# Kernel optimization log

Hardware: AMD Instinct MI355X
Metric: run time of the kernel (lower is better)

The kernel has to match this reference:

```python
import jax, jax.numpy as jnp
import numpy as np

D_MODEL = 2048
N_HEADS = 16
D_HEAD = D_MODEL // N_HEADS
FF = 4 * D_MODEL
ROPE_BASE = 10000.0


def setup_inputs() -> dict:
    key = jax.random.key(0)
    ks = jax.random.split(key, 12)
    s = 0.02
    B, S = 2, 2048
    return {
        "x": jax.random.normal(ks[0], (B, S, D_MODEL), dtype=jnp.float32),
        # torch Linear layout: [out_features, in_features]
        "w_qkv": jax.random.normal(ks[1], (3 * D_MODEL, D_MODEL), dtype=jnp.float32) * s,
        "w_proj": jax.random.normal(ks[2], (D_MODEL, D_MODEL), dtype=jnp.float32) * s,
        "b_proj": jnp.zeros((D_MODEL,), dtype=jnp.float32),
        "w_ff1": jax.random.normal(ks[3], (FF, D_MODEL), dtype=jnp.float32) * s,
        "b_ff1": jnp.zeros((FF,), dtype=jnp.float32),
        "w_ff2": jax.random.normal(ks[4], (D_MODEL, FF), dtype=jnp.float32) * s,
        "b_ff2": jnp.zeros((D_MODEL,), dtype=jnp.float32),
        "g1": jnp.ones((D_MODEL,), dtype=jnp.float32),
        "beta1": jnp.zeros((D_MODEL,), dtype=jnp.float32),
        "g2": jnp.ones((D_MODEL,), dtype=jnp.float32),
        "beta2": jnp.zeros((D_MODEL,), dtype=jnp.float32),
    }


def _layer_norm(x, g, b, eps=1e-5):
    mu = jnp.mean(x, axis=-1, keepdims=True)
    var = jnp.var(x, axis=-1, keepdims=True)
    return (x - mu) * jax.lax.rsqrt(var + eps) * g + b


def _rope_cos_sin(seq_len, dtype):
    inv_freq = 1.0 / (ROPE_BASE ** (jnp.arange(0, D_HEAD, 2, dtype=jnp.float32) / D_HEAD))
    t = jnp.arange(seq_len, dtype=jnp.float32)
    freqs = jnp.einsum("i,j->ij", t, inv_freq)  # [S, D_HEAD//2]
    emb = jnp.concatenate([freqs, freqs], axis=-1)  # [S, D_HEAD]
    return jnp.cos(emb).astype(dtype), jnp.sin(emb).astype(dtype)


def _rotate_half(x):
    x1, x2 = x[..., : D_HEAD // 2], x[..., D_HEAD // 2 :]
    return jnp.concatenate([-x2, x1], axis=-1)


def reference(x, w_qkv, w_proj, b_proj, w_ff1, b_ff1, w_ff2, b_ff2, g1, beta1, g2, beta2):
    B, S, _ = x.shape
    # --- attention block ---
    h = _layer_norm(x, g1, beta1)
    qkv = h @ w_qkv.T  # [B,S,3D]
    xq, xk, xv = jnp.split(qkv, 3, axis=-1)
    xq = xq.reshape(B, S, N_HEADS, D_HEAD)
    xk = xk.reshape(B, S, N_HEADS, D_HEAD)
    xv = xv.reshape(B, S, N_HEADS, D_HEAD)
    cos, sin = _rope_cos_sin(S, x.dtype)
    cos = cos[None, :, None, :]  # [1,S,1,Dh]
    sin = sin[None, :, None, :]
    xq = xq * cos + _rotate_half(xq) * sin
    xk = xk * cos + _rotate_half(xk) * sin
    # SDPA, causal
    scale = 1.0 / jnp.sqrt(jnp.asarray(D_HEAD, dtype=x.dtype))
    scores = jnp.einsum("bqhd,bkhd->bhqk", xq, xk) * scale  # [B,H,S,S]
    causal = jnp.tril(jnp.ones((S, S), dtype=bool))
    scores = jnp.where(causal[None, None], scores, jnp.finfo(x.dtype).min)
    att = jax.nn.softmax(scores, axis=-1)
    out = jnp.einsum("bhqk,bkhd->bqhd", att, xv).reshape(B, S, D_MODEL)
    att_out = out @ w_proj.T + b_proj
    x = x + att_out
    # --- feed-forward block (exact GELU, matching nn.GELU default) ---
    h = _layer_norm(x, g2, beta2)
    ff = jax.nn.gelu(h @ w_ff1.T + b_ff1, approximate=False) @ w_ff2.T + b_ff2
    return x + ff
```

## Files before the change

kernel.cpp:

```cpp
#include <hip/hip_runtime.h>
#include <hip/hip_bf16.h>
#include <cmath>

#define D_MODEL 2048
#define N_HEADS 16
#define D_HEAD  128
#define FFDIM   8192
#define BATCH   2
#define SEQ     2048
#define TOKENS  (BATCH * SEQ)

using bf16 = __hip_bfloat16;
typedef __bf16 v8bf  __attribute__((ext_vector_type(8)));
typedef float  v4f   __attribute__((ext_vector_type(4)));
typedef float  v16f  __attribute__((ext_vector_type(16)));

#define N0 (3 * D_MODEL * D_MODEL / 4)
#define N1 (D_MODEL * D_MODEL / 4)
#define N2 (FFDIM * D_MODEL / 4)
#define N3 (D_MODEL * FFDIM / 4)

__global__ __launch_bounds__(256) void cast4_kernel(const float* __restrict__ w0,
                                                    const float* __restrict__ w1,
                                                    const float* __restrict__ w2,
                                                    const float* __restrict__ w3,
                                                    bf16* __restrict__ o0,
                                                    bf16* __restrict__ o1,
                                                    bf16* __restrict__ o2,
                                                    bf16* __restrict__ o3) {
    int i = blockIdx.x * 256 + threadIdx.x;
    const float* src; bf16* dst; int j;
    if (i < N0)                { src = w0; dst = o0; j = i; }
    else if (i < N0 + N1)      { src = w1; dst = o1; j = i - N0; }
    else if (i < N0 + N1 + N2) { src = w2; dst = o2; j = i - N0 - N1; }
    else                       { src = w3; dst = o3; j = i - N0 - N1 - N2; }
    float4 f = ((const float4*)src)[j];
    int o = j * 4;
    dst[o + 0] = __float2bfloat16(f.x);
    dst[o + 1] = __float2bfloat16(f.y);
    dst[o + 2] = __float2bfloat16(f.z);
    dst[o + 3] = __float2bfloat16(f.w);
}

__global__ __launch_bounds__(256) void ln_kernel(const float* __restrict__ x,
                                                 const float* __restrict__ g,
                                                 const float* __restrict__ b,
                                                 bf16* __restrict__ out) {
    int row = blockIdx.x;
    int t = threadIdx.x;
    const float* xr = x + (size_t)row * D_MODEL;
    float v[8];
    float s = 0.f, s2 = 0.f;
#pragma unroll
    for (int i = 0; i < 8; i++) {
        float val = xr[t + 256 * i];
        v[i] = val;
        s += val;
        s2 += val * val;
    }
#pragma unroll
    for (int off = 32; off > 0; off >>= 1) {
        s  += __shfl_down(s, off, 64);
        s2 += __shfl_down(s2, off, 64);
    }
    __shared__ float ws1[4], ws2[4];
    int wv = t >> 6;
    if ((t & 63) == 0) { ws1[wv] = s; ws2[wv] = s2; }
    __syncthreads();
    float fs  = ws1[0] + ws1[1] + ws1[2] + ws1[3];
    float fs2 = ws2[0] + ws2[1] + ws2[2] + ws2[3];
    float mean = fs * (1.0f / D_MODEL);
    float var  = fs2 * (1.0f / D_MODEL) - mean * mean;
    float rstd = rsqrtf(var + 1e-5f);
    bf16* orow = out + (size_t)row * D_MODEL;
#pragma unroll
    for (int i = 0; i < 8; i++) {
        int c = t + 256 * i;
        orow[c] = __float2bfloat16((v[i] - mean) * rstd * g[c] + b[c]);
    }
}

__global__ __launch_bounds__(256) void rope_kernel(bf16* __restrict__ qkv) {
    int unit = blockIdx.x * 4 + (threadIdx.x >> 6);
    int j = threadIdx.x & 63;
    int h = unit & (N_HEADS - 1);
    int tok = unit >> 4;
    int pos = tok & (SEQ - 1);
    float invf = powf(10000.0f, -(float)j / 64.0f);
    float ang = (float)pos * invf;
    float c = cosf(ang), s = sinf(ang);
    const float sc = 0.08838834764831845f;
    size_t base = (size_t)tok * (3 * D_MODEL) + h * D_HEAD;
    float q1 = __bfloat162float(qkv[base + j]), q2 = __bfloat162float(qkv[base + j + 64]);
    qkv[base + j]      = __float2bfloat16((q1 * c - q2 * s) * sc);
    qkv[base + j + 64] = __float2bfloat16((q2 * c + q1 * s) * sc);
    size_t kb = base + D_MODEL;
    float k1 = __bfloat162float(qkv[kb + j]), k2 = __bfloat162float(qkv[kb + j + 64]);
    qkv[kb + j]      = __float2bfloat16(k1 * c - k2 * s);
    qkv[kb + j + 64] = __float2bfloat16(k2 * c + k1 * s);
}

__global__ __launch_bounds__(256) void vt_kernel(const bf16* __restrict__ qkv,
                                                 bf16* __restrict__ vt) {
    __shared__ float tile[32][65];
    int bh = blockIdx.x;
    int k0 = blockIdx.y * 64;
    int d0 = blockIdx.z * 32;
    int b = bh >> 4, h = bh & 15;
    int t = threadIdx.x;
    const bf16* src = qkv + ((size_t)b * SEQ + k0) * (3 * D_MODEL) + 2 * D_MODEL + h * D_HEAD + d0;
#pragma unroll
    for (int i = 0; i < 8; i++) {
        int e = t + 256 * i;
        int kr = e >> 5, dc = e & 31;
        tile[dc][kr] = __bfloat162float(src[(size_t)kr * (3 * D_MODEL) + dc]);
    }
    __syncthreads();
    bf16* dst = vt + ((size_t)bh * D_HEAD + d0) * SEQ + k0;
#pragma unroll
    for (int i = 0; i < 8; i++) {
        int e = t + 256 * i;
        int dr = e >> 6, kc = e & 63;
        dst[(size_t)dr * SEQ + kc] = __float2bfloat16(tile[dr][kc]);
    }
}

#define KS_STRIDE 136
#define VT_STRIDE 72
#define PS_STRIDE 72

__global__ __launch_bounds__(256) void flash_attn(const bf16* __restrict__ qkv,
                                                  const bf16* __restrict__ vt,
                                                  bf16* __restrict__ att) {
    __shared__ __align__(16) bf16 Ks[64 * KS_STRIDE];
    __shared__ __align__(16) bf16 Vts[D_HEAD * VT_STRIDE];
    __shared__ __align__(16) bf16 Ps[4 * 16 * PS_STRIDE];

    int bh = blockIdx.x;
    int qt = (int)gridDim.y - 1 - (int)blockIdx.y;
    int b = bh >> 4, h = bh & 15;
    int t = threadIdx.x, wave = t >> 6, lane = t & 63;
    int lr = lane & 15, lq = lane >> 4;

    const bf16* qp = qkv + ((size_t)b * SEQ + qt * 64 + wave * 16 + lr) * (3 * D_MODEL) + h * D_HEAD;
    v8bf aq[4];
#pragma unroll
    for (int c = 0; c < 4; c++)
        aq[c] = *(const v8bf*)(qp + c * 32 + lq * 8);

    float m_r[4], l_r[4];
    v4f O[8] = {};
#pragma unroll
    for (int r = 0; r < 4; r++) { m_r[r] = -1e30f; l_r[r] = 0.f; }

    int n_tiles = qt + 1;
    for (int kt = 0; kt < n_tiles; kt++) {
        int kv0 = kt * 64;
        __syncthreads();
        {
            const bf16* kbase = qkv + ((size_t)b * SEQ + kv0) * (3 * D_MODEL) + D_MODEL + h * D_HEAD;
#pragma unroll
            for (int i = 0; i < 4; i++) {
                int e = t + 256 * i;
                int kr = e >> 4, c8 = (e & 15) * 8;
                *(uint4*)&Ks[kr * KS_STRIDE + c8] = *(const uint4*)(kbase + (size_t)kr * (3 * D_MODEL) + c8);
            }
            const bf16* vbase = vt + (size_t)bh * D_HEAD * SEQ + kv0;
#pragma unroll
            for (int i = 0; i < 4; i++) {
                int e8 = t + 256 * i;
                int dr = e8 >> 3, k8 = (e8 & 7) * 8;
                *(uint4*)&Vts[dr * VT_STRIDE + k8] = *(const uint4*)(vbase + (size_t)dr * SEQ + k8);
            }
        }
        __syncthreads();

        v4f sc[4];
#pragma unroll
        for (int nt = 0; nt < 4; nt++) {
            v4f a = {};
#pragma unroll
            for (int c = 0; c < 4; c++) {
                v8bf bk = *(const v8bf*)&Ks[(nt * 16 + lr) * KS_STRIDE + c * 32 + lq * 8];
                a = __builtin_amdgcn_mfma_f32_16x16x32_bf16(aq[c], bk, a, 0, 0, 0);
            }
            sc[nt] = a;
        }
        if (kt == n_tiles - 1) {
#pragma unroll
            for (int nt = 0; nt < 4; nt++)
#pragma unroll
                for (int r = 0; r < 4; r++) {
                    int cl = nt * 16 + lr, rl = wave * 16 + lq * 4 + r;
                    if (cl > rl) sc[nt][r] = -1e30f;
                }
        }
        float mt[4];
#pragma unroll
        for (int r = 0; r < 4; r++) {
            float v = fmaxf(fmaxf(sc[0][r], sc[1][r]), fmaxf(sc[2][r], sc[3][r]));
#pragma unroll
            for (int mk = 8; mk >= 1; mk >>= 1) v = fmaxf(v, __shfl_xor(v, mk, 64));
            mt[r] = v;
        }
        float alpha[4];
#pragma unroll
        for (int r = 0; r < 4; r++) {
            float mn = fmaxf(m_r[r], mt[r]);
            alpha[r] = __expf(m_r[r] - mn);
            m_r[r] = mn;
        }
        bf16* pw = &Ps[wave * 16 * PS_STRIDE];
        float rs[4] = {0.f, 0.f, 0.f, 0.f};
#pragma unroll
        for (int nt = 0; nt < 4; nt++)
#pragma unroll
            for (int r = 0; r < 4; r++) {
                float p = __expf(sc[nt][r] - m_r[r]);
                rs[r] += p;
                pw[(lq * 4 + r) * PS_STRIDE + nt * 16 + lr] = __float2bfloat16(p);
            }
#pragma unroll
        for (int r = 0; r < 4; r++) {
            float v = rs[r];
#pragma unroll
            for (int mk = 8; mk >= 1; mk >>= 1) v += __shfl_xor(v, mk, 64);
            l_r[r] = l_r[r] * alpha[r] + v;
        }
#pragma unroll
        for (int jt = 0; jt < 8; jt++)
#pragma unroll
            for (int r = 0; r < 4; r++) O[jt][r] *= alpha[r];

        asm volatile("s_waitcnt lgkmcnt(0)" ::: "memory");

        v8bf ap[2];
#pragma unroll
        for (int c = 0; c < 2; c++)
            ap[c] = *(const v8bf*)&pw[lr * PS_STRIDE + c * 32 + lq * 8];
#pragma unroll
        for (int jt = 0; jt < 8; jt++) {
#pragma unroll
            for (int c = 0; c < 2; c++) {
                v8bf bv = *(const v8bf*)&Vts[(jt * 16 + lr) * VT_STRIDE + c * 32 + lq * 8];
                O[jt] = __builtin_amdgcn_mfma_f32_16x16x32_bf16(ap[c], bv, O[jt], 0, 0, 0);
            }
        }
    }

    float inv[4];
#pragma unroll
    for (int r = 0; r < 4; r++) inv[r] = 1.0f / l_r[r];
#pragma unroll
    for (int jt = 0; jt < 8; jt++)
#pragma unroll
        for (int r = 0; r < 4; r++) {
            size_t idx = ((size_t)b * SEQ + qt * 64 + wave * 16 + lq * 4 + r) * D_MODEL + h * D_HEAD + jt * 16 + lr;
            att[idx] = __float2bfloat16(O[jt][r] * inv[r]);
        }
}

#define BM 128
#define BN 128
#define BK 64

template <int EPI>
__global__ __launch_bounds__(256) void gemm_bt(const bf16* __restrict__ A,
                                               const bf16* __restrict__ W,
                                               const float* __restrict__ bias,
                                               const float* __restrict__ res,
                                               float* __restrict__ outF,
                                               bf16* __restrict__ outB,
                                               int M, int N, int K) {
    __shared__ __align__(16) bf16 As[BM * BK];
    __shared__ __align__(16) bf16 Bs[BN * BK];
    int t = threadIdx.x;
    int wave = t >> 6, lane = t & 63;
    int wm = (wave >> 1) * 64;
    int wn = (wave & 1) * 64;
    int l31 = lane & 31;
    int kh  = lane >> 5;

    int nbx = gridDim.x;
    int bid = (int)blockIdx.y * nbx + (int)blockIdx.x;
    int per = (nbx * (int)gridDim.y) >> 3;
    int lbid = (bid & 7) * per + (bid >> 3);
    const int GM = 8;
    int pw = GM * nbx;
    int panel = lbid / pw;
    int rem = lbid - panel * pw;
    int bm = panel * GM + (rem & (GM - 1));
    int bn = rem >> 3;
    int row0 = bm * BM;
    int col0 = bn * BN;

    int srow = lane >> 3;
    int sblk = lane & 7;
    int scol = ((sblk ^ srow) * 8);

    v16f acc[2][2] = {};

    for (int k0 = 0; k0 < K; k0 += BK) {
#pragma unroll
        for (int u = 0; u < 4; u++) {
            int c = wave * 4 + u;
            const bf16* ga = A + (size_t)(row0 + c * 8 + srow) * K + k0 + scol;
            __builtin_amdgcn_global_load_lds(
                (const __attribute__((address_space(1))) void*)ga,
                (__attribute__((address_space(3))) void*)&As[c * 512], 16, 0, 0);
            const bf16* gb = W + (size_t)(col0 + c * 8 + srow) * K + k0 + scol;
            __builtin_amdgcn_global_load_lds(
                (const __attribute__((address_space(1))) void*)gb,
                (__attribute__((address_space(3))) void*)&Bs[c * 512], 16, 0, 0);
        }
        __syncthreads();
#pragma unroll
        for (int ks = 0; ks < 4; ks++) {
            int soff = (((ks * 2 + kh) ^ (lane & 7)) * 8);
            v8bf a0 = *(const v8bf*)(&As[(wm +      l31) * BK + soff]);
            v8bf a1 = *(const v8bf*)(&As[(wm + 32 + l31) * BK + soff]);
            v8bf b0 = *(const v8bf*)(&Bs[(wn +      l31) * BK + soff]);
            v8bf b1 = *(const v8bf*)(&Bs[(wn + 32 + l31) * BK + soff]);
            acc[0][0] = __builtin_amdgcn_mfma_f32_32x32x16_bf16(a0, b0, acc[0][0], 0, 0, 0);
            acc[0][1] = __builtin_amdgcn_mfma_f32_32x32x16_bf16(a0, b1, acc[0][1], 0, 0, 0);
            acc[1][0] = __builtin_amdgcn_mfma_f32_32x32x16_bf16(a1, b0, acc[1][0], 0, 0, 0);
            acc[1][1] = __builtin_amdgcn_mfma_f32_32x32x16_bf16(a1, b1, acc[1][1], 0, 0, 0);
        }
        __syncthreads();
    }

#pragma unroll
    for (int ti = 0; ti < 2; ti++) {
#pragma unroll
        for (int tj = 0; tj < 2; tj++) {
#pragma unroll
            for (int reg = 0; reg < 16; reg++) {
                int grow = row0 + wm + ti * 32 + (reg & 3) + 8 * (reg >> 2) + 4 * kh;
                int gcol = col0 + wn + tj * 32 + l31;
                float c = acc[ti][tj][reg];
                size_t idx = (size_t)grow * N + gcol;
                if (EPI == 0) {
                    outF[idx] = c;
                } else if (EPI == 1) {
                    outF[idx] = c + bias[gcol] + res[idx];
                } else if (EPI == 2) {
                    c += bias[gcol];
                    float gel = 0.5f * c * (1.0f + erff(c * 0.7071067811865475f));
                    outB[idx] = __float2bfloat16(gel);
                } else {
                    outB[idx] = __float2bfloat16(c);
                }
            }
        }
    }
}

extern "C" void kernel_launch(void* const* d_in, const int* in_sizes, int n_in,
                              void* d_out, int out_size, void* d_ws, size_t ws_size,
                              hipStream_t stream) {
    const float* x      = (const float*)d_in[0];
    const float* w_qkv  = (const float*)d_in[1];
    const float* w_proj = (const float*)d_in[2];
    const float* b_proj = (const float*)d_in[3];
    const float* w_ff1  = (const float*)d_in[4];
    const float* b_ff1  = (const float*)d_in[5];
    const float* w_ff2  = (const float*)d_in[6];
    const float* b_ff2  = (const float*)d_in[7];
    const float* g1     = (const float*)d_in[8];
    const float* be1    = (const float*)d_in[9];
    const float* g2     = (const float*)d_in[10];
    const float* be2    = (const float*)d_in[11];
    float* out = (float*)d_out;

    char* ws = (char*)d_ws;
    size_t off = 0;
    auto alloc = [&](size_t bytes) {
        void* p = ws + off;
        off += (bytes + 255) & ~(size_t)255;
        return p;
    };
    bf16*  wqkv_b  = (bf16*)alloc((size_t)3 * D_MODEL * D_MODEL * sizeof(bf16));
    bf16*  wproj_b = (bf16*)alloc((size_t)D_MODEL * D_MODEL * sizeof(bf16));
    bf16*  wff1_b  = (bf16*)alloc((size_t)FFDIM * D_MODEL * sizeof(bf16));
    bf16*  wff2_b  = (bf16*)alloc((size_t)D_MODEL * FFDIM * sizeof(bf16));
    bf16*  qkv_b   = (bf16*)alloc((size_t)TOKENS * FFDIM * sizeof(bf16));
    bf16*  ff1_b   = qkv_b;
    bf16*  act_b   = (bf16*)alloc((size_t)TOKENS * D_MODEL * sizeof(bf16));
    float* x2_f    = (float*)alloc((size_t)TOKENS * D_MODEL * sizeof(float));
    bf16*  vt_g    = (bf16*)x2_f;

    cast4_kernel<<<(N0 + N1 + N2 + N3 + 255) / 256, 256, 0, stream>>>(
        w_qkv, w_proj, w_ff1, w_ff2, wqkv_b, wproj_b, wff1_b, wff2_b);

    ln_kernel<<<TOKENS, 256, 0, stream>>>(x, g1, be1, act_b);

    gemm_bt<3><<<dim3(3 * D_MODEL / BN, TOKENS / BM), 256, 0, stream>>>(
        act_b, wqkv_b, nullptr, nullptr, nullptr, qkv_b, TOKENS, 3 * D_MODEL, D_MODEL);

    rope_kernel<<<TOKENS * N_HEADS / 4, 256, 0, stream>>>(qkv_b);

    vt_kernel<<<dim3(BATCH * N_HEADS, SEQ / 64, D_HEAD / 32), 256, 0, stream>>>(qkv_b, vt_g);

    flash_attn<<<dim3(BATCH * N_HEADS, SEQ / 64), 256, 0, stream>>>(qkv_b, vt_g, act_b);

    gemm_bt<1><<<dim3(D_MODEL / BN, TOKENS / BM), 256, 0, stream>>>(
        act_b, wproj_b, b_proj, x, x2_f, nullptr, TOKENS, D_MODEL, D_MODEL);

    ln_kernel<<<TOKENS, 256, 0, stream>>>(x2_f, g2, be2, act_b);

    gemm_bt<2><<<dim3(FFDIM / BN, TOKENS / BM), 256, 0, stream>>>(
        act_b, wff1_b, b_ff1, nullptr, nullptr, ff1_b, TOKENS, FFDIM, D_MODEL);

    gemm_bt<1><<<dim3(D_MODEL / BN, TOKENS / BM), 256, 0, stream>>>(
        ff1_b, wff2_b, b_ff2, x2_f, out, nullptr, TOKENS, D_MODEL, FFDIM);

    (void)in_sizes; (void)n_in; (void)out_size; (void)ws_size;
}
```

Measured before the change: 898.3 us.

## Widen flash attention to 128-query blocks and drop LDS staging in GEMMs

Result: slower. 1.905 ms (+112.1%).

```diff
diff --git a/kernel.cpp b/kernel.cpp
--- a/kernel.cpp
+++ b/kernel.cpp
@@ -129,20 +129,21 @@
 #define VT_STRIDE 72
 #define PS_STRIDE 72
 
-__global__ __launch_bounds__(256) void flash_attn(const bf16* __restrict__ qkv,
+__global__ __launch_bounds__(512) void flash_attn(const bf16* __restrict__ qkv,
                                                   const bf16* __restrict__ vt,
                                                   bf16* __restrict__ att) {
     __shared__ __align__(16) bf16 Ks[64 * KS_STRIDE];
     __shared__ __align__(16) bf16 Vts[D_HEAD * VT_STRIDE];
-    __shared__ __align__(16) bf16 Ps[4 * 16 * PS_STRIDE];
+    __shared__ __align__(16) bf16 Ps[8 * 16 * PS_STRIDE];
 
     int bh = blockIdx.x;
     int qt = (int)gridDim.y - 1 - (int)blockIdx.y;
     int b = bh >> 4, h = bh & 15;
     int t = threadIdx.x, wave = t >> 6, lane = t & 63;
     int lr = lane & 15, lq = lane >> 4;
-
-    const bf16* qp = qkv + ((size_t)b * SEQ + qt * 64 + wave * 16 + lr) * (3 * D_MODEL) + h * D_HEAD;
+    int qbase = qt * 128 + wave * 16;
+
+    const bf16* qp = qkv + ((size_t)b * SEQ + qbase + lr) * (3 * D_MODEL) + h * D_HEAD;
     v8bf aq[4];
 #pragma unroll
     for (int c = 0; c < 4; c++)
@@ -153,27 +154,29 @@
 #pragma unroll
     for (int r = 0; r < 4; r++) { m_r[r] = -1e30f; l_r[r] = 0.f; }
 
-    int n_tiles = qt + 1;
+    int n_tiles = 2 * qt + 2;
+    int ntw = 2 * qt + 1 + (wave >= 4 ? 1 : 0);
     for (int kt = 0; kt < n_tiles; kt++) {
         int kv0 = kt * 64;
         __syncthreads();
         {
             const bf16* kbase = qkv + ((size_t)b * SEQ + kv0) * (3 * D_MODEL) + D_MODEL + h * D_HEAD;
 #pragma unroll
-            for (int i = 0; i < 4; i++) {
-                int e = t + 256 * i;
+            for (int i = 0; i < 2; i++) {
+                int e = t + 512 * i;
                 int kr = e >> 4, c8 = (e & 15) * 8;
                 *(uint4*)&Ks[kr * KS_STRIDE + c8] = *(const uint4*)(kbase + (size_t)kr * (3 * D_MODEL) + c8);
             }
             const bf16* vbase = vt + (size_t)bh * D_HEAD * SEQ + kv0;
 #pragma unroll
-            for (int i = 0; i < 4; i++) {
-                int e8 = t + 256 * i;
+            for (int i = 0; i < 2; i++) {
+                int e8 = t + 512 * i;
                 int dr = e8 >> 3, k8 = (e8 & 7) * 8;
                 *(uint4*)&Vts[dr * VT_STRIDE + k8] = *(const uint4*)(vbase + (size_t)dr * SEQ + k8);
             }
         }
         __syncthreads();
+        if (kt >= ntw) continue;
 
         v4f sc[4];
 #pragma unroll
@@ -186,13 +189,14 @@
             }
             sc[nt] = a;
         }
-        if (kt == n_tiles - 1) {
+        if (kt == ntw - 1) {
 #pragma unroll
             for (int nt = 0; nt < 4; nt++)
 #pragma unroll
                 for (int r = 0; r < 4; r++) {
-                    int cl = nt * 16 + lr, rl = wave * 16 + lq * 4 + r;
-                    if (cl > rl) sc[nt][r] = -1e30f;
+                    int cg = kv0 + nt * 16 + lr;
+                    int rg = qbase + lq * 4 + r;
+                    if (cg > rg) sc[nt][r] = -1e30f;
                 }
         }
         float mt[4];
@@ -255,25 +259,22 @@
     for (int jt = 0; jt < 8; jt++)
 #pragma unroll
         for (int r = 0; r < 4; r++) {
-            size_t idx = ((size_t)b * SEQ + qt * 64 + wave * 16 + lq * 4 + r) * D_MODEL + h * D_HEAD + jt * 16 + lr;
+            size_t idx = ((size_t)b * SEQ + qbase + lq * 4 + r) * D_MODEL + h * D_HEAD + jt * 16 + lr;
             att[idx] = __float2bfloat16(O[jt][r] * inv[r]);
         }
 }
 
 #define BM 128
 #define BN 128
-#define BK 64
 
 template <int EPI>
-__global__ __launch_bounds__(256) void gemm_bt(const bf16* __restrict__ A,
-                                               const bf16* __restrict__ W,
-                                               const float* __restrict__ bias,
-                                               const float* __restrict__ res,
-                                               float* __restrict__ outF,
-                                               bf16* __restrict__ outB,
-                                               int M, int N, int K) {
-    __shared__ __align__(16) bf16 As[BM * BK];
-    __shared__ __align__(16) bf16 Bs[BN * BK];
+__global__ __launch_bounds__(256) void gemm_flat(const bf16* __restrict__ A,
+                                                 const bf16* __restrict__ W,
+                                                 const float* __restrict__ bias,
+                                                 const float* __restrict__ res,
+                                                 float* __restrict__ outF,
+                                                 bf16* __restrict__ outB,
+                                                 int M, int N, int K) {
     int t = threadIdx.x;
     int wave = t >> 6, lane = t & 63;
     int wm = (wave >> 1) * 64;
@@ -294,39 +295,23 @@
     int row0 = bm * BM;
     int col0 = bn * BN;
 
-    int srow = lane >> 3;
-    int sblk = lane & 7;
-    int scol = ((sblk ^ srow) * 8);
+    const bf16* a0p = A + (size_t)(row0 + wm      + l31) * K + kh * 8;
+    const bf16* a1p = A + (size_t)(row0 + wm + 32 + l31) * K + kh * 8;
+    const bf16* b0p = W + (size_t)(col0 + wn      + l31) * K + kh * 8;
+    const bf16* b1p = W + (size_t)(col0 + wn + 32 + l31) * K + kh * 8;
 
     v16f acc[2][2] = {};
 
-    for (int k0 = 0; k0 < K; k0 += BK) {
-#pragma unroll
-        for (int u = 0; u < 4; u++) {
-            int c = wave * 4 + u;
-            const bf16* ga = A + (size_t)(row0 + c * 8 + srow) * K + k0 + scol;
-            __builtin_amdgcn_global_load_lds(
-                (const __attribute__((address_space(1))) void*)ga,
-                (__attribute__((address_space(3))) void*)&As[c * 512], 16, 0, 0);
-            const bf16* gb = W + (size_t)(col0 + c * 8 + srow) * K + k0 + scol;
-            __builtin_amdgcn_global_load_lds(
-                (const __attribute__((address_space(1))) void*)gb,
-                (__attribute__((address_space(3))) void*)&Bs[c * 512], 16, 0, 0);
-        }
-        __syncthreads();
-#pragma unroll
-        for (int ks = 0; ks < 4; ks++) {
-            int soff = (((ks * 2 + kh) ^ (lane & 7)) * 8);
-            v8bf a0 = *(const v8bf*)(&As[(wm +      l31) * BK + soff]);
-            v8bf a1 = *(const v8bf*)(&As[(wm + 32 + l31) * BK + soff]);
-            v8bf b0 = *(const v8bf*)(&Bs[(wn +      l31) * BK + soff]);
-            v8bf b1 = *(const v8bf*)(&Bs[(wn + 32 + l31) * BK + soff]);
-            acc[0][0] = __builtin_amdgcn_mfma_f32_32x32x16_bf16(a0, b0, acc[0][0], 0, 0, 0);
-            acc[0][1] = __builtin_amdgcn_mfma_f32_32x32x16_bf16(a0, b1, acc[0][1], 0, 0, 0);
-            acc[1][0] = __builtin_amdgcn_mfma_f32_32x32x16_bf16(a1, b0, acc[1][0], 0, 0, 0);
-            acc[1][1] = __builtin_amdgcn_mfma_f32_32x32x16_bf16(a1, b1, acc[1][1], 0, 0, 0);
-        }
-        __syncthreads();
+#pragma unroll 4
+    for (int kk = 0; kk < K; kk += 16) {
+        v8bf a0 = *(const v8bf*)(a0p + kk);
+        v8bf a1 = *(const v8bf*)(a1p + kk);
+        v8bf b0 = *(const v8bf*)(b0p + kk);
+        v8bf b1 = *(const v8bf*)(b1p + kk);
+        acc[0][0] = __builtin_amdgcn_mfma_f32_32x32x16_bf16(a0, b0, acc[0][0], 0, 0, 0);
+        acc[0][1] = __builtin_amdgcn_mfma_f32_32x32x16_bf16(a0, b1, acc[0][1], 0, 0, 0);
+        acc[1][0] = __builtin_amdgcn_mfma_f32_32x32x16_bf16(a1, b0, acc[1][0], 0, 0, 0);
+        acc[1][1] = __builtin_amdgcn_mfma_f32_32x32x16_bf16(a1, b1, acc[1][1], 0, 0, 0);
     }
 
 #pragma unroll
@@ -394,24 +379,24 @@
 
     ln_kernel<<<TOKENS, 256, 0, stream>>>(x, g1, be1, act_b);
 
-    gemm_bt<3><<<dim3(3 * D_MODEL / BN, TOKENS / BM), 256, 0, stream>>>(
+    gemm_flat<3><<<dim3(3 * D_MODEL / BN, TOKENS / BM), 256, 0, stream>>>(
         act_b, wqkv_b, nullptr, nullptr, nullptr, qkv_b, TOKENS, 3 * D_MODEL, D_MODEL);
 
     rope_kernel<<<TOKENS * N_HEADS / 4, 256, 0, stream>>>(qkv_b);
 
     vt_kernel<<<dim3(BATCH * N_HEADS, SEQ / 64, D_HEAD / 32), 256, 0, stream>>>(qkv_b, vt_g);
 
-    flash_attn<<<dim3(BATCH * N_HEADS, SEQ / 64), 256, 0, stream>>>(qkv_b, vt_g, act_b);
-
-    gemm_bt<1><<<dim3(D_MODEL / BN, TOKENS / BM), 256, 0, stream>>>(
+    flash_attn<<<dim3(BATCH * N_HEADS, SEQ / 128), 512, 0, stream>>>(qkv_b, vt_g, act_b);
+
+    gemm_flat<1><<<dim3(D_MODEL / BN, TOKENS / BM), 256, 0, stream>>>(
         act_b, wproj_b, b_proj, x, x2_f, nullptr, TOKENS, D_MODEL, D_MODEL);
 
     ln_kernel<<<TOKENS, 256, 0, stream>>>(x2_f, g2, be2, act_b);
 
-    gemm_bt<2><<<dim3(FFDIM / BN, TOKENS / BM), 256, 0, stream>>>(
+    gemm_flat<2><<<dim3(FFDIM / BN, TOKENS / BM), 256, 0, stream>>>(
         act_b, wff1_b, b_ff1, nullptr, nullptr, ff1_b, TOKENS, FFDIM, D_MODEL);
 
-    gemm_bt<1><<<dim3(D_MODEL / BN, TOKENS / BM), 256, 0, stream>>>(
+    gemm_flat<1><<<dim3(D_MODEL / BN, TOKENS / BM), 256, 0, stream>>>(
         ff1_b, wff2_b, b_ff2, x2_f, out, nullptr, TOKENS, D_MODEL, FFDIM);
 
     (void)in_sizes; (void)n_in; (void)out_size; (void)ws_size;
```
